# Optimization experiments

Measured on AMD Instinct MI355X. Metric: run time of the kernel, lower is better.

Reference implementation:

```python
import jax, jax.numpy as jnp
import numpy as np

# Qwen3.5 GatedDeltaNet config (Qwen3-Next linear-attention block)
HIDDEN = 2048
HV, HK = 32, 16          # value heads, key heads (GQA rep = 2)
DK, DV = 128, 128        # key/value head dims
KCONV = 4                # causal depthwise conv kernel
KEY_DIM = HK * DK        # 2048
VAL_DIM = HV * DV        # 4096
CONV_DIM = 2 * KEY_DIM + VAL_DIM  # 8192
EPS = 1e-6


def setup_inputs() -> dict:
    key = jax.random.key(0)
    ks = jax.random.split(key, 9)
    B, S = 2, 1024
    def w(k, shape, sc=0.02):
        return jax.random.normal(k, shape, jnp.float32) * sc
    return {
        "hidden_states": jax.random.normal(ks[0], (B, S, HIDDEN), jnp.float32),
        "conv_w": w(ks[1], (CONV_DIM, 1, KCONV), 0.1),   # depthwise conv1d weight (groups=CONV_DIM, no bias)
        "w_qkv": w(ks[2], (HIDDEN, CONV_DIM)),
        "w_z": w(ks[3], (HIDDEN, VAL_DIM)),
        "w_b": w(ks[4], (HIDDEN, HV)),
        "w_a": w(ks[5], (HIDDEN, HV)),
        "w_out": w(ks[6], (VAL_DIM, HIDDEN)),
        "dt_bias": jnp.ones((HV,), jnp.float32),
        "A_log": jnp.log(jax.random.uniform(ks[7], (HV,), jnp.float32, 1e-3, 16.0)),
        "norm_w": jnp.ones((DV,), jnp.float32),
    }


def _l2norm(x):
    return x / jnp.sqrt(jnp.sum(x * x, axis=-1, keepdims=True) + 1e-6)


def reference(hidden_states, conv_w, w_qkv, w_z, w_b, w_a, w_out, dt_bias, A_log, norm_w):
    B, S, _ = hidden_states.shape
    # input projections
    mixed = hidden_states @ w_qkv                     # [B,S,CONV_DIM]
    z = (hidden_states @ w_z).reshape(B, S, HV, DV)   # gate for RMSNormGated
    b = hidden_states @ w_b                           # [B,S,HV]
    a = hidden_states @ w_a                           # [B,S,HV]

    # causal depthwise conv1d (left pad K-1), then SiLU
    x = mixed.transpose(0, 2, 1)                      # [B,C,S]
    y = jax.lax.conv_general_dilated(
        x, conv_w, window_strides=(1,), padding=[(KCONV - 1, 0)],
        dimension_numbers=("NCH", "OIH", "NCH"), feature_group_count=CONV_DIM)
    mixed = jax.nn.silu(y).transpose(0, 2, 1)         # [B,S,CONV_DIM]

    q, k, v = jnp.split(mixed, [KEY_DIM, 2 * KEY_DIM], axis=-1)
    q = q.reshape(B, S, HK, DK)
    k = k.reshape(B, S, HK, DK)
    v = v.reshape(B, S, HV, DV)

    beta = jax.nn.sigmoid(b)                                    # [B,S,HV]
    g = -jnp.exp(A_log) * jax.nn.softplus(a + dt_bias)          # [B,S,HV], log-decay <= 0

    rep = HV // HK
    q = jnp.repeat(q, rep, axis=2)                              # [B,S,HV,DK]
    k = jnp.repeat(k, rep, axis=2)

    # use_qk_l2norm_in_kernel=True, then standard 1/sqrt(dk) scaling on q
    q = _l2norm(q) * (DK ** -0.5)
    k = _l2norm(k)

    # gated delta-rule recurrence over time (state S: [B,HV,DK,DV])
    qt = q.transpose(1, 0, 2, 3)
    kt = k.transpose(1, 0, 2, 3)
    vt = v.transpose(1, 0, 2, 3)
    gt = g.transpose(1, 0, 2)
    bt = beta.transpose(1, 0, 2)

    S0 = jnp.zeros((B, HV, DK, DV), jnp.float32)

    def step(Sm, inp):
        q_, k_, v_, g_, b_ = inp
        Sm = Sm * jnp.exp(g_)[..., None, None]                  # gated decay
        kv = jnp.einsum('bhk,bhkv->bhv', k_, Sm)                # k^T S (current memory readout)
        delta = (v_ - kv) * b_[..., None]                       # delta-rule update, scaled by beta
        Sm = Sm + jnp.einsum('bhk,bhv->bhkv', k_, delta)        # rank-1 write
        o = jnp.einsum('bhk,bhkv->bhv', q_, Sm)                 # query readout
        return Sm, o

    _, o = jax.lax.scan(step, S0, (qt, kt, vt, gt, bt))
    o = o.transpose(1, 0, 2, 3)                                 # [B,S,HV,DV]

    # RMSNormGated over head_v_dim: gate with silu(z), then RMSNorm
    og = o * jax.nn.silu(z)
    var = jnp.mean(og * og, axis=-1, keepdims=True)
    on = og * jax.lax.rsqrt(var + EPS) * norm_w

    return on.reshape(B, S, VAL_DIM) @ w_out                    # [B,S,HIDDEN]
```

## Files before the change

### kernel.cpp

```cpp
#include <hip/hip_runtime.h>
#include <hip/hip_bf16.h>
#include <cstdint>

#define HIDDEN   2048
#define HV       32
#define HK       16
#define DK       128
#define DV       128
#define KEY_DIM  2048
#define VAL_DIM  4096
#define CONV_DIM 8192
#define NTOK     2048
#define SEQ      1024
#define N1       12288
#define C_CH     64
#define NCHK     (SEQ / C_CH)

typedef __attribute__((ext_vector_type(4))) float f4_t;
typedef __attribute__((ext_vector_type(2))) float f2_t;
typedef __attribute__((ext_vector_type(8))) short bf8_t;
typedef __attribute__((ext_vector_type(16))) float f16acc;
typedef __attribute__((ext_vector_type(4))) unsigned short u16x4;
typedef __attribute__((ext_vector_type(8))) unsigned short u16x8;
typedef __attribute__((ext_vector_type(2))) uint32_t u32x2;
typedef __attribute__((ext_vector_type(4))) uint32_t u32x4;

__device__ __forceinline__ unsigned short f2bf(float f) {
    union { float f; uint32_t u; } a; a.f = f;
    uint32_t u = a.u;
    return (unsigned short)((u + 0x7fff + ((u >> 16) & 1)) >> 16);
}
__device__ __forceinline__ float bf2f(unsigned short h) {
    uint32_t u = ((uint32_t)h) << 16;
    union { uint32_t u; float f; } a; a.u = u;
    return a.f;
}
__device__ __forceinline__ bf8_t lds_frag(const unsigned short* p) {
    u32x2 a = *(const u32x2*)p;
    u32x2 b = *(const u32x2*)(p + 4);
    u32x4 w = {a[0], a[1], b[0], b[1]};
    return __builtin_bit_cast(bf8_t, w);
}

__global__ __launch_bounds__(256) void k_cast_hs(const float* __restrict__ hs,
                                                 unsigned short* __restrict__ out) {
    int i = blockIdx.x * 256 + threadIdx.x;
    f4_t v = ((const f4_t*)hs)[i];
    u16x4 o;
    o[0] = f2bf(v[0]); o[1] = f2bf(v[1]); o[2] = f2bf(v[2]); o[3] = f2bf(v[3]);
    ((u16x4*)out)[i] = o;
}

__global__ __launch_bounds__(256) void k_trans_w1(const float* __restrict__ w_qkv,
                                                  const float* __restrict__ w_z,
                                                  unsigned short* __restrict__ w1t) {
    __shared__ float tile[32][33];
    int tx = threadIdx.x & 31, ty = threadIdx.x >> 5;
    int n0 = blockIdx.x * 32, k0 = blockIdx.y * 32;
    int n = n0 + tx;
#pragma unroll
    for (int i = 0; i < 4; i++) {
        int k = k0 + ty + i * 8;
        float v = (n < CONV_DIM) ? w_qkv[(size_t)k * CONV_DIM + n]
                                 : w_z[(size_t)k * VAL_DIM + (n - CONV_DIM)];
        tile[ty + i * 8][tx] = v;
    }
    __syncthreads();
#pragma unroll
    for (int i = 0; i < 4; i++)
        w1t[(size_t)(n0 + ty + i * 8) * HIDDEN + k0 + tx] = f2bf(tile[tx][ty + i * 8]);
}

__global__ __launch_bounds__(256) void k_trans(const float* __restrict__ src,
                                               unsigned short* __restrict__ dst,
                                               int K, int N) {
    __shared__ float tile[32][33];
    int tx = threadIdx.x & 31, ty = threadIdx.x >> 5;
    int n0 = blockIdx.x * 32, k0 = blockIdx.y * 32;
#pragma unroll
    for (int i = 0; i < 4; i++)
        tile[ty + i * 8][tx] = src[(size_t)(k0 + ty + i * 8) * N + n0 + tx];
    __syncthreads();
#pragma unroll
    for (int i = 0; i < 4; i++)
        dst[(size_t)(n0 + ty + i * 8) * K + k0 + tx] = f2bf(tile[tx][ty + i * 8]);
}

__global__ __launch_bounds__(256, 4) void k_gemm_bt(const unsigned short* __restrict__ A,
                                                    const unsigned short* __restrict__ B,
                                                    float* __restrict__ C, int K, int N) {
    __shared__ unsigned short lA[2][128 * 32];
    __shared__ unsigned short lB[2][128 * 32];
    int tid = threadIdx.x;
    int wave = tid >> 6, lane = tid & 63;
    int nwg = gridDim.x * gridDim.y;
    int lid = blockIdx.y * gridDim.x + blockIdx.x;
    int swz = (lid & 7) * (nwg >> 3) + (lid >> 3);
    int m0 = (swz & 15) * 128, n0 = (swz >> 4) * 128;
    int wm = wave & 1, wn = wave >> 1;
    f4_t acc[4][4];
#pragma unroll
    for (int i = 0; i < 4; i++)
#pragma unroll
        for (int j = 0; j < 4; j++) acc[i][j] = (f4_t){0.f, 0.f, 0.f, 0.f};
    int srow = wave * 16 + (lane >> 2);
    int scol = ((lane & 3) ^ ((lane >> 3) & 3)) * 8;
    int quad = lane >> 4, lrow = lane & 15;
    int rswz = (lrow >> 1) & 3;

    const unsigned short* gA0 = A + (size_t)(m0 + srow) * K + scol;
    const unsigned short* gA1 = A + (size_t)(m0 + 64 + srow) * K + scol;
    const unsigned short* gB0 = B + (size_t)(n0 + srow) * K + scol;
    const unsigned short* gB1 = B + (size_t)(n0 + 64 + srow) * K + scol;

#define GEMM_STAGE(buf, k0)                                                                        \
    do {                                                                                           \
        __builtin_amdgcn_global_load_lds((const __attribute__((address_space(1))) void*)(gA0 + (k0)), \
            (__attribute__((address_space(3))) void*)(&lA[buf][wave * 512]), 16, 0, 0);            \
        __builtin_amdgcn_global_load_lds((const __attribute__((address_space(1))) void*)(gA1 + (k0)), \
            (__attribute__((address_space(3))) void*)(&lA[buf][2048 + wave * 512]), 16, 0, 0);     \
        __builtin_amdgcn_global_load_lds((const __attribute__((address_space(1))) void*)(gB0 + (k0)), \
            (__attribute__((address_space(3))) void*)(&lB[buf][wave * 512]), 16, 0, 0);            \
        __builtin_amdgcn_global_load_lds((const __attribute__((address_space(1))) void*)(gB1 + (k0)), \
            (__attribute__((address_space(3))) void*)(&lB[buf][2048 + wave * 512]), 16, 0, 0);     \
    } while (0)

    GEMM_STAGE(0, 0);
    __syncthreads();

    int cur = 0;
    for (int k0 = 0; k0 < K; k0 += 32) {
        if (k0 + 32 < K) GEMM_STAGE(cur ^ 1, k0 + 32);
        bf8_t af[4], bfv[4];
#pragma unroll
        for (int i = 0; i < 4; i++) {
            int sa = (quad ^ rswz) * 8;
            af[i]  = *(const bf8_t*)&lA[cur][(wm * 64 + i * 16 + lrow) * 32 + sa];
            bfv[i] = *(const bf8_t*)&lB[cur][(wn * 64 + i * 16 + lrow) * 32 + sa];
        }
#pragma unroll
        for (int i = 0; i < 4; i++)
#pragma unroll
            for (int j = 0; j < 4; j++)
                acc[i][j] = __builtin_amdgcn_mfma_f32_16x16x32_bf16(af[i], bfv[j], acc[i][j], 0, 0, 0);
        __syncthreads();
        cur ^= 1;
    }
#undef GEMM_STAGE
#pragma unroll
    for (int i = 0; i < 4; i++) {
        int row_b = m0 + wm * 64 + i * 16 + quad * 4;
#pragma unroll
        for (int j = 0; j < 4; j++) {
            int col = n0 + wn * 64 + j * 16 + lrow;
#pragma unroll
            for (int r = 0; r < 4; r++)
                C[(size_t)(row_b + r) * N + col] = acc[i][j][r];
        }
    }
}

#define BG_TOK 4
__global__ __launch_bounds__(256) void k_beta_g(const float* __restrict__ hs,
                                                const float* __restrict__ w_b,
                                                const float* __restrict__ w_a,
                                                const float* __restrict__ dt_bias,
                                                const float* __restrict__ A_log,
                                                float* __restrict__ beta,
                                                float* __restrict__ gval) {
    __shared__ float rows[BG_TOK * HIDDEN];
    __shared__ float part[BG_TOK][64][17];
    int t = threadIdx.x;
    int tok0 = blockIdx.x * BG_TOK;
    {
        const f4_t* src = (const f4_t*)(hs + (size_t)tok0 * HIDDEN);
        f4_t* dst = (f4_t*)rows;
#pragma unroll
        for (int u = 0; u < BG_TOK * HIDDEN / 4 / 256; u++)
            dst[t + u * 256] = src[t + u * 256];
    }
    __syncthreads();
    int hq = t & 15, kp = t >> 4;
    int h0 = hq * 4;
    const float* wsrc = (h0 < 32) ? (w_b + h0) : (w_a + (h0 - 32));
    f4_t acc[BG_TOK];
#pragma unroll
    for (int x = 0; x < BG_TOK; x++) acc[x] = (f4_t){0.f, 0.f, 0.f, 0.f};
    int kbase = kp * 128;
#pragma unroll 4
    for (int i = 0; i < 128; i++) {
        int k = kbase + i;
        f4_t wv = *(const f4_t*)(wsrc + (size_t)k * 32);
#pragma unroll
        for (int x = 0; x < BG_TOK; x++) {
            float r = rows[x * HIDDEN + k];
            acc[x][0] += wv[0] * r;
            acc[x][1] += wv[1] * r;
            acc[x][2] += wv[2] * r;
            acc[x][3] += wv[3] * r;
        }
    }
#pragma unroll
    for (int x = 0; x < BG_TOK; x++)
#pragma unroll
        for (int e = 0; e < 4; e++)
            part[x][h0 + e][kp] = acc[x][e];
    __syncthreads();
    int x = t >> 6, h = t & 63;
    float s = 0.f;
#pragma unroll
    for (int k2 = 0; k2 < 16; k2++) s += part[x][h][k2];
    int tok = tok0 + x;
    if (h < 32) {
        beta[tok * 32 + h] = 1.f / (1.f + expf(-s));
    } else {
        int hh = h - 32;
        float xx = s + dt_bias[hh];
        float sp = (xx > 20.f) ? xx : log1pf(expf(xx));
        gval[tok * 32 + hh] = -expf(A_log[hh]) * sp;
    }
}

#define CCH 32
#define NCHC (SEQ / CCH)
__global__ __launch_bounds__(256) void k_halo(const float* __restrict__ mixed,
                                              float* __restrict__ halo) {
    int id = blockIdx.x * 256 + threadIdx.x;
    int c = id & 8191;
    int r = id >> 13;
    int tap = r % 3;
    int ck = (r / 3) % (NCHC - 1);
    int b = r / (3 * (NCHC - 1));
    int s = (ck + 1) * CCH - 1 - tap;
    halo[id] = mixed[(size_t)(b * SEQ + s) * N1 + c];
}

__global__ __launch_bounds__(256) void k_conv(float* __restrict__ mixed,
                                              const float* __restrict__ cw,
                                              const float* __restrict__ halo) {
    int id = blockIdx.x * 256 + threadIdx.x;
    int c = id & 8191;
    int r = id >> 13;
    int chunk = r & (NCHC - 1), b = r >> 5;
    int s0 = chunk * CCH;
    float w0 = cw[c * 4 + 0], w1 = cw[c * 4 + 1], w2 = cw[c * 4 + 2], w3 = cw[c * 4 + 3];
    float xm1, xm2, xm3;
    if (chunk == 0) {
        xm1 = xm2 = xm3 = 0.f;
    } else {
        const float* hp = halo + (size_t)(b * (NCHC - 1) + chunk - 1) * 3 * 8192;
        xm1 = hp[0 * 8192 + c]; xm2 = hp[1 * 8192 + c]; xm3 = hp[2 * 8192 + c];
    }
    float* col = mixed + (size_t)(b * SEQ + s0) * N1 + c;
#pragma unroll
    for (int s = 0; s < CCH; s++) {
        float x = col[(size_t)s * N1];
        float y = w3 * x + w2 * xm1 + w1 * xm2 + w0 * xm3;
        y = y / (1.f + expf(-y));
        col[(size_t)s * N1] = y;
        xm3 = xm2; xm2 = xm1; xm1 = x;
    }
}

__global__ __launch_bounds__(256) void k_l2norm(float* __restrict__ mixed) {
    int tok = blockIdx.x, t = threadIdx.x;
    int vec = t >> 3, ln = t & 7;
    int off = (vec < 16) ? vec * 128 : 2048 + (vec - 16) * 128;
    float* p = mixed + (size_t)tok * N1 + off + ln * 16;
    f4_t x0 = ((f4_t*)p)[0], x1 = ((f4_t*)p)[1], x2 = ((f4_t*)p)[2], x3 = ((f4_t*)p)[3];
    float ss = 0.f;
#pragma unroll
    for (int i = 0; i < 4; i++) ss += x0[i]*x0[i] + x1[i]*x1[i] + x2[i]*x2[i] + x3[i]*x3[i];
    ss += __shfl_xor(ss, 1); ss += __shfl_xor(ss, 2); ss += __shfl_xor(ss, 4);
    float sc = 1.f / sqrtf(ss + 1e-6f);
    if (vec < 16) sc *= 0.08838834764831845f;
#pragma unroll
    for (int i = 0; i < 4; i++) { x0[i]*=sc; x1[i]*=sc; x2[i]*=sc; x3[i]*=sc; }
    ((f4_t*)p)[0] = x0; ((f4_t*)p)[1] = x1; ((f4_t*)p)[2] = x2; ((f4_t*)p)[3] = x3;
}

__global__ __launch_bounds__(256, 2) void k_prep(const float* __restrict__ mixed,
                                                 const float* __restrict__ beta,
                                                 const float* __restrict__ gval,
                                                 unsigned short* __restrict__ Pg,
                                                 unsigned short* __restrict__ KbTg,
                                                 unsigned short* __restrict__ Qbg,
                                                 unsigned short* __restrict__ Wg,
                                                 float* __restrict__ Ug,
                                                 float* __restrict__ Lamg) {
    __shared__ unsigned short lK[64 * 132];
    __shared__ unsigned short lQ[64 * 132];
    __shared__ float lM[64 * 66];
    __shared__ float lG[64], lLam[64], lBeta[64], lKsc[64];

    int blk = blockIdx.x;
    int c = blk & 15, h = (blk >> 4) & 31, b = blk >> 9;
    int hk = h >> 1;
    int t = threadIdx.x;
    int wave = t >> 6, lane = t & 63, half = lane >> 5, lm = lane & 31;
    int s0 = c * C_CH;

    const float* qptr = mixed + (size_t)(b * SEQ) * N1 + hk * 128;
    const float* kptr = qptr + 2048;

    {
        int i = t >> 2, c0 = (t & 3) * 32;
        const float* kr = kptr + (size_t)(s0 + i) * N1 + c0;
        const float* qr = qptr + (size_t)(s0 + i) * N1 + c0;
        unsigned short* dK = &lK[i * 132 + c0];
        unsigned short* dQ = &lQ[i * 132 + c0];
#pragma unroll
        for (int u = 0; u < 8; u++) {
            f4_t kv = ((const f4_t*)kr)[u];
            f4_t qv = ((const f4_t*)qr)[u];
            u16x4 ks, qs;
#pragma unroll
            for (int e = 0; e < 4; e++) { ks[e] = f2bf(kv[e]); qs[e] = f2bf(qv[e]); }
            *(u16x4*)(dK + u * 4) = ks;
            *(u16x4*)(dQ + u * 4) = qs;
        }
        if (t < 64) {
            float gv = gval[(size_t)(b * SEQ + s0 + t) * 32 + h];
            float bv = beta[(size_t)(b * SEQ + s0 + t) * 32 + h];
            float x = gv;
#pragma unroll
            for (int d = 1; d < 64; d <<= 1) {
                float y = __shfl_up(x, d);
                if (t >= d) x += y;
            }
            float Gc = __shfl(x, 63);
            lG[t] = x; lLam[t] = expf(x); lBeta[t] = bv; lKsc[t] = expf(Gc - x);
        }
    }
    __syncthreads();

    size_t bhc = (size_t)(b * 32 + h) * 16 + c;
    size_t bkc = (size_t)(b * 16 + hk) * 16 + c;

    for (int job = wave; job < 6; job += 4) {
        int isP = job >= 3 ? 1 : 0;
        int jj = job - (isP ? 3 : 0);
        int ib = (jj == 0) ? 0 : 1;
        int jb = (jj == 2) ? 1 : 0;
        const unsigned short* Ab = isP ? lQ : lK;
        f16acc acc;
#pragma unroll
        for (int r = 0; r < 16; r++) acc[r] = 0.f;
        int arow = ib * 32 + lm, brow = jb * 32 + lm;
#pragma unroll
        for (int k0 = 0; k0 < 128; k0 += 16) {
            bf8_t a = lds_frag(&Ab[arow * 132 + k0 + half * 8]);
            bf8_t bb = lds_frag(&lK[brow * 132 + k0 + half * 8]);
            acc = __builtin_amdgcn_mfma_f32_32x32x16_bf16(a, bb, acc, 0, 0, 0);
        }
        int j = jb * 32 + lm;
        float Gj = lG[j];
#pragma unroll
        for (int r = 0; r < 16; r++) {
            int ml = (r & 3) + 8 * (r >> 2) + 4 * half;
            int i = ib * 32 + ml;
            float f = expf(lG[i] - Gj);
            if (isP) {
                Pg[bhc * 4096 + i * 64 + j] = f2bf((j <= i) ? acc[r] * f : 0.f);
            } else {
                if (j < i) lM[i * 66 + j] = acc[r] * lBeta[i] * f;
            }
        }
    }
#pragma unroll
    for (int u = 0; u < 4; u++) {
        int e = t * 4 + u;
        Pg[bhc * 4096 + (e >> 5) * 64 + 32 + (e & 31)] = 0;
    }

    if ((h & 1) == 0) {
        int i = t >> 2, c0 = (t & 3) * 32;
#pragma unroll
        for (int u = 0; u < 8; u++)
            *(u16x4*)&Qbg[bkc * 8192 + i * 128 + c0 + u * 4] = *(const u16x4*)&lQ[i * 132 + c0 + u * 4];
    }

    {
        int dk = t >> 1, i0 = (t & 1) * 32;
        unsigned short tmp[32];
#pragma unroll
        for (int ii = 0; ii < 32; ii++) {
            int i = i0 + ii;
            tmp[ii] = f2bf(bf2f(lK[i * 132 + dk]) * lKsc[i]);
        }
#pragma unroll
        for (int u = 0; u < 4; u++) {
            u16x8 w;
#pragma unroll
            for (int j = 0; j < 8; j++) w[j] = tmp[u * 8 + j];
            *(u16x8*)&KbTg[bhc * 8192 + dk * 64 + i0 + u * 8] = w;
        }
    }
    if (t < 64) Lamg[bhc * 64 + t] = lLam[t];

    __syncthreads();

    {
        float x[64];
        if (t < 128) {
            const float* vcol = mixed + (size_t)(b * SEQ + s0) * N1 + 4096 + h * 128 + t;
#pragma unroll
            for (int il = 0; il < 64; il++) x[il] = lBeta[il] * vcol[(size_t)il * N1];
        } else {
            int dk = t - 128;
#pragma unroll
            for (int il = 0; il < 64; il++) x[il] = lBeta[il] * lLam[il] * bf2f(lK[il * 132 + dk]);
        }
#pragma unroll
        for (int il = 1; il < 64; il++)
#pragma unroll
            for (int j = 0; j < il; j++)
                x[il] -= lM[il * 66 + j] * x[j];
        if (t < 128) {
            float* up = Ug + (size_t)(b * SEQ + s0) * 4096 + h * 128 + t;
#pragma unroll
            for (int il = 0; il < 64; il++) up[(size_t)il * 4096] = x[il];
        } else {
            unsigned short* wp = Wg + bhc * 8192 + (t - 128);
#pragma unroll
            for (int il = 0; il < 64; il++) wp[il * 128] = f2bf(-x[il]);
        }
    }
}

__global__ __launch_bounds__(256, 1) void k_state(const unsigned short* __restrict__ Wg,
                                                  const unsigned short* __restrict__ Pg,
                                                  const unsigned short* __restrict__ KbTg,
                                                  const unsigned short* __restrict__ Qbg,
                                                  const float* __restrict__ Lamg,
                                                  float* __restrict__ o) {
    __shared__ unsigned short lSt[32 * 132];
    __shared__ unsigned short lDt[32 * 68];

    int blk = blockIdx.x;
    int vs = blk & 3, h = (blk >> 2) & 31, b = blk >> 7;
    int hk = h >> 1;
    int t = threadIdx.x;
    int wave = t >> 6, lane = t & 63, half = lane >> 5, lm = lane & 31;
    int ib = wave & 1;

    for (int i = t; i < 32 * 132; i += 256) lSt[i] = 0;
    f16acc sacc;
#pragma unroll
    for (int r = 0; r < 16; r++) sacc[r] = 0.f;
    __syncthreads();

    for (int c = 0; c < NCHK; c++) {
        int s0 = c * C_CH;
        size_t bhc = (size_t)(b * 32 + h) * 16 + c;
        size_t bkc = (size_t)(b * 16 + hk) * 16 + c;

        const unsigned short* Ag = (wave < 2) ? (Wg + bhc * 8192) : (Qbg + bkc * 8192);
        bf8_t afr[8];
#pragma unroll
        for (int kk = 0; kk < 8; kk++)
            afr[kk] = *(const bf8_t*)&Ag[(ib * 32 + lm) * 128 + kk * 16 + half * 8];
        bf8_t ktfr[4];
#pragma unroll
        for (int u = 0; u < 4; u++)
            ktfr[u] = *(const bf8_t*)&KbTg[bhc * 8192 + (wave * 32 + lm) * 64 + u * 16 + half * 8];
        bf8_t pfr[4];
        f4_t lamv[4];
        if (wave >= 2) {
#pragma unroll
            for (int u = 0; u < 4; u++)
                pfr[u] = *(const bf8_t*)&Pg[bhc * 4096 + (ib * 32 + lm) * 64 + u * 16 + half * 8];
#pragma unroll
            for (int q = 0; q < 4; q++)
                lamv[q] = *(const f4_t*)&Lamg[bhc * 64 + ib * 32 + q * 8 + half * 4];
        }
        float lamC = Lamg[bhc * 64 + 63];

        f16acc wacc;
        if (wave < 2) {
            const float* up = o + (size_t)(b * SEQ + s0 + ib * 32) * 4096 + h * 128 + vs * 32 + lm;
#pragma unroll
            for (int r = 0; r < 16; r++) {
                int ml = (r & 3) + 8 * (r >> 2) + 4 * half;
                wacc[r] = up[(size_t)ml * 4096];
            }
        } else {
#pragma unroll
            for (int r = 0; r < 16; r++) wacc[r] = 0.f;
        }
#pragma unroll
        for (int kk = 0; kk < 8; kk++) {
            bf8_t bb = lds_frag(&lSt[lm * 132 + kk * 16 + half * 8]);
            wacc = __builtin_amdgcn_mfma_f32_32x32x16_bf16(afr[kk], bb, wacc, 0, 0, 0);
        }
        if (wave < 2) {
#pragma unroll
            for (int r = 0; r < 16; r++) {
                int ml = (r & 3) + 8 * (r >> 2) + 4 * half;
                lDt[lm * 68 + ib * 32 + ml] = f2bf(wacc[r]);
            }
        }
        __syncthreads();

        if (wave >= 2) {
#pragma unroll
            for (int r = 0; r < 16; r++) wacc[r] *= lamv[r >> 2][r & 3];
#pragma unroll
            for (int u = 0; u < 4; u++) {
                bf8_t bb = lds_frag(&lDt[lm * 68 + u * 16 + half * 8]);
                wacc = __builtin_amdgcn_mfma_f32_32x32x16_bf16(pfr[u], bb, wacc, 0, 0, 0);
            }
#pragma unroll
            for (int r = 0; r < 16; r++) {
                int ml = (r & 3) + 8 * (r >> 2) + 4 * half;
                o[(size_t)(b * SEQ + s0 + ib * 32 + ml) * 4096 + h * 128 + vs * 32 + lm] = wacc[r];
            }
        }
#pragma unroll
        for (int r = 0; r < 16; r++) sacc[r] *= lamC;
#pragma unroll
        for (int u = 0; u < 4; u++) {
            bf8_t bb = lds_frag(&lDt[lm * 68 + u * 16 + half * 8]);
            sacc = __builtin_amdgcn_mfma_f32_32x32x16_bf16(ktfr[u], bb, sacc, 0, 0, 0);
        }
#pragma unroll
        for (int r = 0; r < 16; r++) {
            int ml = (r & 3) + 8 * (r >> 2) + 4 * half;
            lSt[lm * 132 + 32 * wave + ml] = f2bf(sacc[r]);
        }
        __syncthreads();
    }
}

__global__ __launch_bounds__(256) void k_gnorm(const float* __restrict__ o,
                                               const float* __restrict__ mixed,
                                               const float* __restrict__ norm_w,
                                               unsigned short* __restrict__ on) {
    int tok = blockIdx.x, t = threadIdx.x;
    int hh = t >> 3, ln = t & 7;
    const f4_t* op = (const f4_t*)(o + (size_t)tok * 4096 + hh * 128 + ln * 16);
    const f4_t* zp = (const f4_t*)(mixed + (size_t)tok * N1 + 8192 + hh * 128 + ln * 16);
    float og[16];
    float ss = 0.f;
#pragma unroll
    for (int i = 0; i < 4; i++) {
        f4_t ov = op[i], zv = zp[i];
#pragma unroll
        for (int j = 0; j < 4; j++) {
            float z = zv[j];
            float g = ov[j] * (z / (1.f + expf(-z)));
            og[i * 4 + j] = g;
            ss += g * g;
        }
    }
    ss += __shfl_xor(ss, 1); ss += __shfl_xor(ss, 2); ss += __shfl_xor(ss, 4);
    float r = 1.f / sqrtf(ss * (1.f / 128.f) + 1e-6f);
    unsigned short* onp = on + (size_t)tok * 4096 + hh * 128 + ln * 16;
    u16x8 a, bb;
#pragma unroll
    for (int j = 0; j < 8; j++) a[j] = f2bf(og[j] * r * norm_w[ln * 16 + j]);
#pragma unroll
    for (int j = 0; j < 8; j++) bb[j] = f2bf(og[8 + j] * r * norm_w[ln * 16 + 8 + j]);
    ((u16x8*)onp)[0] = a;
    ((u16x8*)onp)[1] = bb;
}

extern "C" void kernel_launch(void* const* d_in, const int* in_sizes, int n_in,
                              void* d_out, int out_size, void* d_ws, size_t ws_size,
                              hipStream_t stream) {
    const float* hs      = (const float*)d_in[0];
    const float* conv_w  = (const float*)d_in[1];
    const float* w_qkv   = (const float*)d_in[2];
    const float* w_z     = (const float*)d_in[3];
    const float* w_b     = (const float*)d_in[4];
    const float* w_a     = (const float*)d_in[5];
    const float* w_out   = (const float*)d_in[6];
    const float* dt_bias = (const float*)d_in[7];
    const float* A_log   = (const float*)d_in[8];
    const float* norm_w  = (const float*)d_in[9];
    float* out = (float*)d_out;

    char* ws = (char*)d_ws;
    unsigned short* hs_bf = (unsigned short*)ws; ws += (size_t)NTOK * HIDDEN * 2;
    unsigned short* w1t   = (unsigned short*)ws; ws += (size_t)N1 * HIDDEN * 2;
    unsigned short* wot   = (unsigned short*)ws; ws += (size_t)HIDDEN * VAL_DIM * 2;
    float* mixed          = (float*)ws;          ws += (size_t)NTOK * N1 * 4;
    float* beta           = (float*)ws;          ws += (size_t)NTOK * 32 * 4;
    float* gval           = (float*)ws;          ws += (size_t)NTOK * 32 * 4;
    float* halo           = (float*)ws;          ws += (size_t)2 * (NCHC - 1) * 3 * 8192 * 4;
    float* o_buf          = (float*)ws;          ws += (size_t)NTOK * VAL_DIM * 4;
    unsigned short* on_bf = (unsigned short*)ws; ws += (size_t)NTOK * VAL_DIM * 2;

    char* al = (char*)hs_bf;
    unsigned short* Wg    = (unsigned short*)al; al += (size_t)1024 * 8192 * 2;
    unsigned short* Pg    = (unsigned short*)al; al += (size_t)1024 * 4096 * 2;
    unsigned short* KbTg  = (unsigned short*)al; al += (size_t)1024 * 8192 * 2;
    unsigned short* Qbg   = (unsigned short*)al; al += (size_t)512 * 8192 * 2;
    float* Lamg           = (float*)halo;

    k_cast_hs<<<dim3(NTOK * HIDDEN / 4 / 256), 256, 0, stream>>>(hs, hs_bf);
    k_trans_w1<<<dim3(N1 / 32, HIDDEN / 32), 256, 0, stream>>>(w_qkv, w_z, w1t);
    k_trans<<<dim3(HIDDEN / 32, VAL_DIM / 32), 256, 0, stream>>>(w_out, wot, VAL_DIM, HIDDEN);
    k_gemm_bt<<<dim3(NTOK / 128, N1 / 128), 256, 0, stream>>>(hs_bf, w1t, mixed, HIDDEN, N1);
    k_beta_g<<<dim3(NTOK / BG_TOK), 256, 0, stream>>>(hs, w_b, w_a, dt_bias, A_log, beta, gval);
    k_halo<<<dim3(2 * (NCHC - 1) * 3 * 8192 / 256), 256, 0, stream>>>(mixed, halo);
    k_conv<<<dim3(2 * NCHC * 8192 / 256), 256, 0, stream>>>(mixed, conv_w, halo);
    k_l2norm<<<dim3(NTOK), 256, 0, stream>>>(mixed);
    k_prep<<<dim3(1024), 256, 0, stream>>>(mixed, beta, gval, Pg, KbTg, Qbg, Wg, o_buf, Lamg);
    k_state<<<dim3(256), 256, 0, stream>>>(Wg, Pg, KbTg, Qbg, Lamg, o_buf);
    k_gnorm<<<dim3(NTOK), 256, 0, stream>>>(o_buf, mixed, norm_w, on_bf);
    k_gemm_bt<<<dim3(NTOK / 128, HIDDEN / 128), 256, 0, stream>>>(on_bf, wot, out, VAL_DIM, HIDDEN);
}
```

Baseline: 572.8 us.

## Store projected qkv/z in bf16 and fuse L2 norm into chunk prep

The first projection GEMM now writes bf16 instead of fp32 for the mixed buffer. The conv writes q/k back as bf16 and v to a separate fp32 buffer. The standalone L2-norm kernel is removed and its work is folded into k_prep, which normalizes q and k rows while loading them. This roughly halves the traffic on the large intermediate and drops one launch plus a full read/write pass. In exchange, the conv input and z are rounded to bf16 before the conv and the gate, which adds precision loss.

```diff
diff --git a/kernel.cpp b/kernel.cpp
--- a/kernel.cpp
+++ b/kernel.cpp
@@ -1,6 +1,7 @@
 #include <hip/hip_runtime.h>
 #include <hip/hip_bf16.h>
 #include <cstdint>
+#include <type_traits>
 
 #define HIDDEN   2048
 #define HV       32
@@ -86,9 +87,10 @@
         dst[(size_t)(n0 + ty + i * 8) * K + k0 + tx] = f2bf(tile[tx][ty + i * 8]);
 }
 
+template <typename OT>
 __global__ __launch_bounds__(256, 4) void k_gemm_bt(const unsigned short* __restrict__ A,
                                                     const unsigned short* __restrict__ B,
-                                                    float* __restrict__ C, int K, int N) {
+                                                    OT* __restrict__ C, int K, int N) {
     __shared__ unsigned short lA[2][128 * 32];
     __shared__ unsigned short lB[2][128 * 32];
     int tid = threadIdx.x;
@@ -154,8 +156,12 @@
         for (int j = 0; j < 4; j++) {
             int col = n0 + wn * 64 + j * 16 + lrow;
 #pragma unroll
-            for (int r = 0; r < 4; r++)
-                C[(size_t)(row_b + r) * N + col] = acc[i][j][r];
+            for (int r = 0; r < 4; r++) {
+                if constexpr (std::is_same<OT, float>::value)
+                    C[(size_t)(row_b + r) * N + col] = acc[i][j][r];
+                else
+                    C[(size_t)(row_b + r) * N + col] = f2bf(acc[i][j][r]);
+            }
         }
     }
 }
@@ -223,8 +229,8 @@
 
 #define CCH 32
 #define NCHC (SEQ / CCH)
-__global__ __launch_bounds__(256) void k_halo(const float* __restrict__ mixed,
-                                              float* __restrict__ halo) {
+__global__ __launch_bounds__(256) void k_halo(const unsigned short* __restrict__ mixed,
+                                              unsigned short* __restrict__ halo) {
     int id = blockIdx.x * 256 + threadIdx.x;
     int c = id & 8191;
     int r = id >> 13;
@@ -235,9 +241,10 @@
     halo[id] = mixed[(size_t)(b * SEQ + s) * N1 + c];
 }
 
-__global__ __launch_bounds__(256) void k_conv(float* __restrict__ mixed,
+__global__ __launch_bounds__(256) void k_conv(unsigned short* __restrict__ mixed,
                                               const float* __restrict__ cw,
-                                              const float* __restrict__ halo) {
+                                              const unsigned short* __restrict__ halo,
+                                              float* __restrict__ vbuf) {
     int id = blockIdx.x * 256 + threadIdx.x;
     int c = id & 8191;
     int r = id >> 13;
@@ -248,38 +255,24 @@
     if (chunk == 0) {
         xm1 = xm2 = xm3 = 0.f;
     } else {
-        const float* hp = halo + (size_t)(b * (NCHC - 1) + chunk - 1) * 3 * 8192;
-        xm1 = hp[0 * 8192 + c]; xm2 = hp[1 * 8192 + c]; xm3 = hp[2 * 8192 + c];
-    }
-    float* col = mixed + (size_t)(b * SEQ + s0) * N1 + c;
+        const unsigned short* hp = halo + (size_t)(b * (NCHC - 1) + chunk - 1) * 3 * 8192;
+        xm1 = bf2f(hp[0 * 8192 + c]); xm2 = bf2f(hp[1 * 8192 + c]); xm3 = bf2f(hp[2 * 8192 + c]);
+    }
+    unsigned short* col = mixed + (size_t)(b * SEQ + s0) * N1 + c;
+    float* vcol = vbuf + (size_t)(b * SEQ + s0) * 4096 + (c - 4096);
 #pragma unroll
     for (int s = 0; s < CCH; s++) {
-        float x = col[(size_t)s * N1];
+        float x = bf2f(col[(size_t)s * N1]);
         float y = w3 * x + w2 * xm1 + w1 * xm2 + w0 * xm3;
         y = y / (1.f + expf(-y));
-        col[(size_t)s * N1] = y;
+        if (c < 4096) col[(size_t)s * N1] = f2bf(y);
+        else          vcol[(size_t)s * 4096] = y;
         xm3 = xm2; xm2 = xm1; xm1 = x;
     }
 }
 
-__global__ __launch_bounds__(256) void k_l2norm(float* __restrict__ mixed) {
-    int tok = blockIdx.x, t = threadIdx.x;
-    int vec = t >> 3, ln = t & 7;
-    int off = (vec < 16) ? vec * 128 : 2048 + (vec - 16) * 128;
-    float* p = mixed + (size_t)tok * N1 + off + ln * 16;
-    f4_t x0 = ((f4_t*)p)[0], x1 = ((f4_t*)p)[1], x2 = ((f4_t*)p)[2], x3 = ((f4_t*)p)[3];
-    float ss = 0.f;
-#pragma unroll
-    for (int i = 0; i < 4; i++) ss += x0[i]*x0[i] + x1[i]*x1[i] + x2[i]*x2[i] + x3[i]*x3[i];
-    ss += __shfl_xor(ss, 1); ss += __shfl_xor(ss, 2); ss += __shfl_xor(ss, 4);
-    float sc = 1.f / sqrtf(ss + 1e-6f);
-    if (vec < 16) sc *= 0.08838834764831845f;
-#pragma unroll
-    for (int i = 0; i < 4; i++) { x0[i]*=sc; x1[i]*=sc; x2[i]*=sc; x3[i]*=sc; }
-    ((f4_t*)p)[0] = x0; ((f4_t*)p)[1] = x1; ((f4_t*)p)[2] = x2; ((f4_t*)p)[3] = x3;
-}
-
-__global__ __launch_bounds__(256, 2) void k_prep(const float* __restrict__ mixed,
+__global__ __launch_bounds__(256, 2) void k_prep(const unsigned short* __restrict__ mixed,
+                                                 const float* __restrict__ vbuf,
                                                  const float* __restrict__ beta,
                                                  const float* __restrict__ gval,
                                                  unsigned short* __restrict__ Pg,
@@ -300,24 +293,52 @@
     int wave = t >> 6, lane = t & 63, half = lane >> 5, lm = lane & 31;
     int s0 = c * C_CH;
 
-    const float* qptr = mixed + (size_t)(b * SEQ) * N1 + hk * 128;
-    const float* kptr = qptr + 2048;
+    const unsigned short* qptr = mixed + (size_t)(b * SEQ) * N1 + hk * 128;
+    const unsigned short* kptr = qptr + 2048;
 
     {
         int i = t >> 2, c0 = (t & 3) * 32;
-        const float* kr = kptr + (size_t)(s0 + i) * N1 + c0;
-        const float* qr = qptr + (size_t)(s0 + i) * N1 + c0;
-        unsigned short* dK = &lK[i * 132 + c0];
-        unsigned short* dQ = &lQ[i * 132 + c0];
-#pragma unroll
-        for (int u = 0; u < 8; u++) {
-            f4_t kv = ((const f4_t*)kr)[u];
-            f4_t qv = ((const f4_t*)qr)[u];
-            u16x4 ks, qs;
-#pragma unroll
-            for (int e = 0; e < 4; e++) { ks[e] = f2bf(kv[e]); qs[e] = f2bf(qv[e]); }
-            *(u16x4*)(dK + u * 4) = ks;
-            *(u16x4*)(dQ + u * 4) = qs;
+        {
+            const unsigned short* kr = kptr + (size_t)(s0 + i) * N1 + c0;
+            float kv[32];
+            float ssk = 0.f;
+#pragma unroll
+            for (int u = 0; u < 4; u++) {
+                u16x8 w = *(const u16x8*)(kr + u * 8);
+#pragma unroll
+                for (int e = 0; e < 8; e++) { float f = bf2f(w[e]); kv[u * 8 + e] = f; ssk += f * f; }
+            }
+            ssk += __shfl_xor(ssk, 1); ssk += __shfl_xor(ssk, 2);
+            float sck = 1.f / sqrtf(ssk + 1e-6f);
+            unsigned short* dK = &lK[i * 132 + c0];
+#pragma unroll
+            for (int u = 0; u < 8; u++) {
+                u16x4 s4;
+#pragma unroll
+                for (int e = 0; e < 4; e++) s4[e] = f2bf(kv[u * 4 + e] * sck);
+                *(u16x4*)(dK + u * 4) = s4;
+            }
+        }
+        {
+            const unsigned short* qr = qptr + (size_t)(s0 + i) * N1 + c0;
+            float qv[32];
+            float ssq = 0.f;
+#pragma unroll
+            for (int u = 0; u < 4; u++) {
+                u16x8 w = *(const u16x8*)(qr + u * 8);
+#pragma unroll
+                for (int e = 0; e < 8; e++) { float f = bf2f(w[e]); qv[u * 8 + e] = f; ssq += f * f; }
+            }
+            ssq += __shfl_xor(ssq, 1); ssq += __shfl_xor(ssq, 2);
+            float scq = (1.f / sqrtf(ssq + 1e-6f)) * 0.08838834764831845f;
+            unsigned short* dQ = &lQ[i * 132 + c0];
+#pragma unroll
+            for (int u = 0; u < 8; u++) {
+                u16x4 s4;
+#pragma unroll
+                for (int e = 0; e < 4; e++) s4[e] = f2bf(qv[u * 4 + e] * scq);
+                *(u16x4*)(dQ + u * 4) = s4;
+            }
         }
         if (t < 64) {
             float gv = gval[(size_t)(b * SEQ + s0 + t) * 32 + h];
@@ -403,9 +424,9 @@
     {
         float x[64];
         if (t < 128) {
-            const float* vcol = mixed + (size_t)(b * SEQ + s0) * N1 + 4096 + h * 128 + t;
-#pragma unroll
-            for (int il = 0; il < 64; il++) x[il] = lBeta[il] * vcol[(size_t)il * N1];
+            const float* vcol = vbuf + (size_t)(b * SEQ + s0) * 4096 + h * 128 + t;
+#pragma unroll
+            for (int il = 0; il < 64; il++) x[il] = lBeta[il] * vcol[(size_t)il * 4096];
         } else {
             int dk = t - 128;
 #pragma unroll
@@ -533,23 +554,26 @@
 }
 
 __global__ __launch_bounds__(256) void k_gnorm(const float* __restrict__ o,
-                                               const float* __restrict__ mixed,
+                                               const unsigned short* __restrict__ mixed,
                                                const float* __restrict__ norm_w,
                                                unsigned short* __restrict__ on) {
     int tok = blockIdx.x, t = threadIdx.x;
     int hh = t >> 3, ln = t & 7;
     const f4_t* op = (const f4_t*)(o + (size_t)tok * 4096 + hh * 128 + ln * 16);
-    const f4_t* zp = (const f4_t*)(mixed + (size_t)tok * N1 + 8192 + hh * 128 + ln * 16);
+    const unsigned short* zp = mixed + (size_t)tok * N1 + 8192 + hh * 128 + ln * 16;
+    u16x8 zr0 = *(const u16x8*)zp;
+    u16x8 zr1 = *(const u16x8*)(zp + 8);
     float og[16];
     float ss = 0.f;
 #pragma unroll
     for (int i = 0; i < 4; i++) {
-        f4_t ov = op[i], zv = zp[i];
+        f4_t ov = op[i];
 #pragma unroll
         for (int j = 0; j < 4; j++) {
-            float z = zv[j];
+            int e = i * 4 + j;
+            float z = (e < 8) ? bf2f(zr0[e]) : bf2f(zr1[e - 8]);
             float g = ov[j] * (z / (1.f + expf(-z)));
-            og[i * 4 + j] = g;
+            og[e] = g;
             ss += g * g;
         }
     }
@@ -584,10 +608,11 @@
     unsigned short* hs_bf = (unsigned short*)ws; ws += (size_t)NTOK * HIDDEN * 2;
     unsigned short* w1t   = (unsigned short*)ws; ws += (size_t)N1 * HIDDEN * 2;
     unsigned short* wot   = (unsigned short*)ws; ws += (size_t)HIDDEN * VAL_DIM * 2;
-    float* mixed          = (float*)ws;          ws += (size_t)NTOK * N1 * 4;
+    unsigned short* mixed = (unsigned short*)ws; ws += (size_t)NTOK * N1 * 2;
+    float* vbuf           = (float*)ws;          ws += (size_t)NTOK * 4096 * 4;
     float* beta           = (float*)ws;          ws += (size_t)NTOK * 32 * 4;
     float* gval           = (float*)ws;          ws += (size_t)NTOK * 32 * 4;
-    float* halo           = (float*)ws;          ws += (size_t)2 * (NCHC - 1) * 3 * 8192 * 4;
+    unsigned short* halo  = (unsigned short*)ws; ws += (size_t)2 * (NCHC - 1) * 3 * 8192 * 2;
     float* o_buf          = (float*)ws;          ws += (size_t)NTOK * VAL_DIM * 4;
     unsigned short* on_bf = (unsigned short*)ws; ws += (size_t)NTOK * VAL_DIM * 2;
 
@@ -601,13 +626,12 @@
     k_cast_hs<<<dim3(NTOK * HIDDEN / 4 / 256), 256, 0, stream>>>(hs, hs_bf);
     k_trans_w1<<<dim3(N1 / 32, HIDDEN / 32), 256, 0, stream>>>(w_qkv, w_z, w1t);
     k_trans<<<dim3(HIDDEN / 32, VAL_DIM / 32), 256, 0, stream>>>(w_out, wot, VAL_DIM, HIDDEN);
-    k_gemm_bt<<<dim3(NTOK / 128, N1 / 128), 256, 0, stream>>>(hs_bf, w1t, mixed, HIDDEN, N1);
+    k_gemm_bt<unsigned short><<<dim3(NTOK / 128, N1 / 128), 256, 0, stream>>>(hs_bf, w1t, mixed, HIDDEN, N1);
     k_beta_g<<<dim3(NTOK / BG_TOK), 256, 0, stream>>>(hs, w_b, w_a, dt_bias, A_log, beta, gval);
     k_halo<<<dim3(2 * (NCHC - 1) * 3 * 8192 / 256), 256, 0, stream>>>(mixed, halo);
-    k_conv<<<dim3(2 * NCHC * 8192 / 256), 256, 0, stream>>>(mixed, conv_w, halo);
-    k_l2norm<<<dim3(NTOK), 256, 0, stream>>>(mixed);
-    k_prep<<<dim3(1024), 256, 0, stream>>>(mixed, beta, gval, Pg, KbTg, Qbg, Wg, o_buf, Lamg);
+    k_conv<<<dim3(2 * NCHC * 8192 / 256), 256, 0, stream>>>(mixed, conv_w, halo, vbuf);
+    k_prep<<<dim3(1024), 256, 0, stream>>>(mixed, vbuf, beta, gval, Pg, KbTg, Qbg, Wg, o_buf, Lamg);
     k_state<<<dim3(256), 256, 0, stream>>>(Wg, Pg, KbTg, Qbg, Lamg, o_buf);
     k_gnorm<<<dim3(NTOK), 256, 0, stream>>>(o_buf, mixed, norm_w, on_bf);
-    k_gemm_bt<<<dim3(NTOK / 128, HIDDEN / 128), 256, 0, stream>>>(on_bf, wot, out, VAL_DIM, HIDDEN);
-}
+    k_gemm_bt<float><<<dim3(NTOK / 128, HIDDEN / 128), 256, 0, stream>>>(on_bf, wot, out, VAL_DIM, HIDDEN);
+}
```

After: 552.9 us. -3.5%, faster.
